# Optimization experiments

Measured on AMD Instinct MI355X. Metric: run time of the kernel, lower is better.

Reference implementation:

```python
import jax, jax.numpy as jnp
import numpy as np


def setup_inputs() -> dict:
    key = jax.random.key(0)
    k0, k1, k2, k3 = jax.random.split(key, 4)
    B, C_IN, H, W = 8, 256, 64, 64
    O, NUM = 256, 8  # output channels, number of regions
    mat0 = jax.random.normal(k0, (B, C_IN, H, W), dtype=jnp.float32)
    mat1 = jax.random.normal(k1, (O, C_IN, NUM), dtype=jnp.float32)  # per-region 1x1 filters (shared across batch, batch_W=1)
    mask = jax.random.uniform(k2, (NUM, H, W), dtype=jnp.float32)    # soft region weights per pixel
    Alpha = jax.random.uniform(k3, (NUM,), dtype=jnp.float32)        # per-region modulation scale
    return {"mat0": mat0, "mat1": mat1, "mask": mask, "Alpha": Alpha, "use_alpha": 1, "beta": 1}


def reference(mat0, mat1, mask, Alpha, use_alpha, beta):
    # Deformable (region-aware) matmul: for each pixel (h,w), apply the
    # region-r filter mat1[:, :, r] to mat0[:, :, h, w], weighted by the
    # per-pixel soft region mask (optionally alpha-modulated per region).
    # out[b,o,h,w] = sum_r sum_c mat0[b,c,h,w] * mat1[o,c,r] * Alpha[r] * mask[r,h,w]
    m1 = mat1 * Alpha if use_alpha else mat1  # [O, C, R] scaled per region
    return jnp.einsum('bchw,ocr,rhw->bohw', mat0, m1, mask)
```

## Files before the change

kernel.cpp:

```cpp
#include <hip/hip_runtime.h>
#include <hip/hip_bf16.h>
#include <stdint.h>


typedef __attribute__((ext_vector_type(8))) short short8;
typedef __attribute__((ext_vector_type(4))) float f32x4;

#define C_IN  256
#define HW_   4096
#define O_DIM 256
#define BM    128
#define BN    128
#define NRND  32

__device__ __forceinline__ short f2bf(float x) {
  union { __hip_bfloat16 h; short s; } u;
  u.h = __float2bfloat16(x);
  return u.s;
}

__global__ __launch_bounds__(256) void prep_w_kernel(
    const float* __restrict__ mat1, const float* __restrict__ Alpha,
    const int* __restrict__ use_alpha, short* __restrict__ Aprep) {
  int t = blockIdx.x * 256 + threadIdx.x;
  int o = t & 255;
  int c = t >> 8;
  int ua = use_alpha[0];
  const float* src = mat1 + ((size_t)o * C_IN + c) * 8;
  short8 v;
#pragma unroll
  for (int r = 0; r < 8; ++r) {
    float s = ua ? Alpha[r] : 1.0f;
    v[r] = f2bf(src[r] * s);
  }
  *(short8*)(Aprep + ((size_t)c * 256 + o) * 8) = v;
}

__global__ __launch_bounds__(256, 2) void gemm_deform_kernel(
    const float* __restrict__ mat0, const short* __restrict__ Aprep,
    const float* __restrict__ mask, float* __restrict__ out) {
  int bid = blockIdx.x;
  int wg = (bid & 7) * 64 + (bid >> 3);
  int tile_m = wg & 1;
  int tile_n = wg >> 1;
  int o0 = tile_m * BM;
  int n0 = tile_n * BN;
  int b  = n0 >> 12;
  int p0 = n0 & 4095;

  int t    = threadIdx.x;
  int lane = t & 63;
  int w    = t >> 6;
  int wr   = w >> 1, wc = w & 1;
  int kp   = lane >> 4;
  int li   = lane & 15;

  int colb = p0 + wc * 64 + li;
  float mk[4][8];
#pragma unroll
  for (int ni = 0; ni < 4; ++ni)
#pragma unroll
    for (int r = 0; r < 8; ++r)
      mk[ni][r] = mask[r * HW_ + colb + ni * 16];

  const short8* __restrict__ Ap = (const short8*)Aprep;
  int abase0 = kp * 256 + o0 + wr * 64 + li;

  const float* __restrict__ m0 = mat0 + ((size_t)b * C_IN + kp) * HW_ + colb;

  f32x4 acc[4][4];
#pragma unroll
  for (int mi = 0; mi < 4; ++mi)
#pragma unroll
    for (int ni = 0; ni < 4; ++ni) acc[mi][ni] = (f32x4){0.f, 0.f, 0.f, 0.f};

  short8 afA[2][4], afB[2][4];
  float  m0A[2][4], m0B[2][4];

  auto LOAD = [&](short8 (&af)[2][4], float (&m0v)[2][4], int rd) {
    int ab = rd * 8 * 256 + abase0;
#pragma unroll
    for (int ks = 0; ks < 2; ++ks)
#pragma unroll
      for (int mi = 0; mi < 4; ++mi)
        af[ks][mi] = Ap[ab + ks * 4 * 256 + mi * 16];
    const float* mp = m0 + (size_t)(rd * 8) * HW_;
#pragma unroll
    for (int ks = 0; ks < 2; ++ks)
#pragma unroll
      for (int ni = 0; ni < 4; ++ni)
        m0v[ks][ni] = mp[(size_t)(ks * 4) * HW_ + ni * 16];
  };

  auto COMP = [&](const short8 (&af)[2][4], const float (&m0v)[2][4]) {
#pragma unroll
    for (int ks = 0; ks < 2; ++ks) {
      short8 bv[4];
#pragma unroll
      for (int ni = 0; ni < 4; ++ni)
#pragma unroll
        for (int r = 0; r < 8; ++r)
          bv[ni][r] = f2bf(m0v[ks][ni] * mk[ni][r]);
#pragma unroll
      for (int mi = 0; mi < 4; ++mi)
#pragma unroll
        for (int ni = 0; ni < 4; ++ni)
          acc[mi][ni] = __builtin_amdgcn_mfma_f32_16x16x32_bf16(
              af[ks][mi], bv[ni], acc[mi][ni], 0, 0, 0);
    }
  };

  LOAD(afA, m0A, 0);
#pragma unroll 1
  for (int rd = 0; rd < NRND; rd += 2) {
    LOAD(afB, m0B, rd + 1);
    COMP(afA, m0A);
    if (rd + 2 < NRND) LOAD(afA, m0A, rd + 2);
    COMP(afB, m0B);
  }

  size_t obase = (size_t)b * O_DIM * HW_ + p0;
#pragma unroll
  for (int mi = 0; mi < 4; ++mi) {
#pragma unroll
    for (int ni = 0; ni < 4; ++ni) {
      int col = wc * 64 + ni * 16 + li;
#pragma unroll
      for (int j = 0; j < 4; ++j) {
        int row = o0 + wr * 64 + mi * 16 + kp * 4 + j;
        out[obase + (size_t)row * HW_ + col] = acc[mi][ni][j];
      }
    }
  }
}

extern "C" void kernel_launch(void* const* d_in, const int* in_sizes, int n_in,
                              void* d_out, int out_size, void* d_ws, size_t ws_size,
                              hipStream_t stream) {
  const float* mat0      = (const float*)d_in[0];
  const float* mat1      = (const float*)d_in[1];
  const float* mask      = (const float*)d_in[2];
  const float* Alpha     = (const float*)d_in[3];
  const int*   use_alpha = (const int*)d_in[4];
  (void)in_sizes; (void)n_in; (void)out_size; (void)ws_size;

  short* Aprep = (short*)d_ws;
  float* outp  = (float*)d_out;

  prep_w_kernel<<<256, 256, 0, stream>>>(mat1, Alpha, use_alpha, Aprep);
  gemm_deform_kernel<<<512, 256, 0, stream>>>(mat0, Aprep, mask, outp);
}
```

Baseline: 53.27 us.

## Split K across wave pairs with 32x32 MFMA and LDS reduction

The GEMM block grows from 256 to 512 threads. Each pair of waves splits the K dimension and uses 32x32x16 bf16 MFMAs in place of 16x16x32, with partial sums combined through shared memory before the store. This roughly halves per-wave accumulator and register pressure and doubles the waves available to hide latency. It adds a 64KB LDS reduction buffer and a block-wide barrier, and the large LDS footprint may limit how many blocks fit per CU.

```diff
diff --git a/kernel.cpp b/kernel.cpp
--- a/kernel.cpp
+++ b/kernel.cpp
@@ -3,8 +3,9 @@
 #include <stdint.h>
 
 
-typedef __attribute__((ext_vector_type(8))) short short8;
-typedef __attribute__((ext_vector_type(4))) float f32x4;
+typedef __attribute__((ext_vector_type(8)))  short short8;
+typedef __attribute__((ext_vector_type(4)))  float f32x4;
+typedef __attribute__((ext_vector_type(16))) float f32x16;
 
 #define C_IN  256
 #define HW_   4096
@@ -36,9 +37,11 @@
   *(short8*)(Aprep + ((size_t)c * 256 + o) * 8) = v;
 }
 
-__global__ __launch_bounds__(256, 2) void gemm_deform_kernel(
+__global__ __launch_bounds__(512, 4) void gemm_deform_kernel(
     const float* __restrict__ mat0, const short* __restrict__ Aprep,
     const float* __restrict__ mask, float* __restrict__ out) {
+  __shared__ float red[8 * 2048];
+
   int bid = blockIdx.x;
   int wg = (bid & 7) * 64 + (bid >> 3);
   int tile_m = wg & 1;
@@ -51,62 +54,67 @@
   int t    = threadIdx.x;
   int lane = t & 63;
   int w    = t >> 6;
-  int wr   = w >> 1, wc = w & 1;
-  int kp   = lane >> 4;
-  int li   = lane & 15;
+  int wk   = w & 1;
+  int wc   = (w >> 1) & 1;
+  int wr   = w >> 2;
+  int l31  = lane & 31;
+  int cr   = lane >> 5;
 
-  int colb = p0 + wc * 64 + li;
-  float mk[4][8];
+  int colb = p0 + wc * 64 + l31;
+  float mk[2][8];
 #pragma unroll
-  for (int ni = 0; ni < 4; ++ni)
+  for (int ni = 0; ni < 2; ++ni)
 #pragma unroll
     for (int r = 0; r < 8; ++r)
-      mk[ni][r] = mask[r * HW_ + colb + ni * 16];
+      mk[ni][r] = mask[r * HW_ + colb + ni * 32];
 
   const short8* __restrict__ Ap = (const short8*)Aprep;
-  int abase0 = kp * 256 + o0 + wr * 64 + li;
+  int abase0 = (wk * 4 + cr) * 256 + o0 + wr * 64 + l31;
 
-  const float* __restrict__ m0 = mat0 + ((size_t)b * C_IN + kp) * HW_ + colb;
+  const float* __restrict__ m0 =
+      mat0 + ((size_t)b * C_IN + wk * 4 + cr) * HW_ + colb;
 
-  f32x4 acc[4][4];
+  f32x16 acc[2][2];
 #pragma unroll
-  for (int mi = 0; mi < 4; ++mi)
+  for (int mi = 0; mi < 2; ++mi)
 #pragma unroll
-    for (int ni = 0; ni < 4; ++ni) acc[mi][ni] = (f32x4){0.f, 0.f, 0.f, 0.f};
+    for (int ni = 0; ni < 2; ++ni)
+#pragma unroll
+      for (int j = 0; j < 16; ++j) acc[mi][ni][j] = 0.f;
 
-  short8 afA[2][4], afB[2][4];
-  float  m0A[2][4], m0B[2][4];
+  short8 afA[2][2], afB[2][2];
+  float  m0A[2][2], m0B[2][2];
 
-  auto LOAD = [&](short8 (&af)[2][4], float (&m0v)[2][4], int rd) {
+  auto LOAD = [&](short8 (&af)[2][2], float (&m0v)[2][2], int rd) {
     int ab = rd * 8 * 256 + abase0;
 #pragma unroll
-    for (int ks = 0; ks < 2; ++ks)
+    for (int kq = 0; kq < 2; ++kq)
 #pragma unroll
-      for (int mi = 0; mi < 4; ++mi)
-        af[ks][mi] = Ap[ab + ks * 4 * 256 + mi * 16];
+      for (int mi = 0; mi < 2; ++mi)
+        af[kq][mi] = Ap[ab + kq * 2 * 256 + mi * 32];
     const float* mp = m0 + (size_t)(rd * 8) * HW_;
 #pragma unroll
-    for (int ks = 0; ks < 2; ++ks)
+    for (int kq = 0; kq < 2; ++kq)
 #pragma unroll
-      for (int ni = 0; ni < 4; ++ni)
-        m0v[ks][ni] = mp[(size_t)(ks * 4) * HW_ + ni * 16];
+      for (int ni = 0; ni < 2; ++ni)
+        m0v[kq][ni] = mp[(size_t)(kq * 2) * HW_ + ni * 32];
   };
 
-  auto COMP = [&](const short8 (&af)[2][4], const float (&m0v)[2][4]) {
+  auto COMP = [&](const short8 (&af)[2][2], const float (&m0v)[2][2]) {
 #pragma unroll
-    for (int ks = 0; ks < 2; ++ks) {
-      short8 bv[4];
+    for (int kq = 0; kq < 2; ++kq) {
+      short8 bv[2];
 #pragma unroll
-      for (int ni = 0; ni < 4; ++ni)
+      for (int ni = 0; ni < 2; ++ni)
 #pragma unroll
         for (int r = 0; r < 8; ++r)
-          bv[ni][r] = f2bf(m0v[ks][ni] * mk[ni][r]);
+          bv[ni][r] = f2bf(m0v[kq][ni] * mk[ni][r]);
 #pragma unroll
-      for (int mi = 0; mi < 4; ++mi)
+      for (int mi = 0; mi < 2; ++mi)
 #pragma unroll
-        for (int ni = 0; ni < 4; ++ni)
-          acc[mi][ni] = __builtin_amdgcn_mfma_f32_16x16x32_bf16(
-              af[ks][mi], bv[ni], acc[mi][ni], 0, 0, 0);
+        for (int ni = 0; ni < 2; ++ni)
+          acc[mi][ni] = __builtin_amdgcn_mfma_f32_32x32x16_bf16(
+              af[kq][mi], bv[ni], acc[mi][ni], 0, 0, 0);
     }
   };
 
@@ -119,17 +127,36 @@
     COMP(afB, m0B);
   }
 
+  int pairid = wr * 2 + wc;
+  int other  = wk ^ 1;
+  float* reg_w = &red[(pairid * 2 + other) * 2048];
+#pragma unroll
+  for (int ni = 0; ni < 2; ++ni)
+#pragma unroll
+    for (int q = 0; q < 4; ++q) {
+      f32x4 v;
+#pragma unroll
+      for (int j = 0; j < 4; ++j) v[j] = acc[other][ni][q * 4 + j];
+      *(f32x4*)&reg_w[(q * 128 + ni * 64 + lane) * 4] = v;
+    }
+  __syncthreads();
+
+  const float* reg_r = &red[(pairid * 2 + wk) * 2048];
   size_t obase = (size_t)b * O_DIM * HW_ + p0;
 #pragma unroll
-  for (int mi = 0; mi < 4; ++mi) {
+  for (int ni = 0; ni < 2; ++ni) {
+    f32x16 s = acc[wk][ni];
 #pragma unroll
-    for (int ni = 0; ni < 4; ++ni) {
-      int col = wc * 64 + ni * 16 + li;
+    for (int q = 0; q < 4; ++q) {
+      f32x4 v = *(const f32x4*)&reg_r[(q * 128 + ni * 64 + lane) * 4];
 #pragma unroll
-      for (int j = 0; j < 4; ++j) {
-        int row = o0 + wr * 64 + mi * 16 + kp * 4 + j;
-        out[obase + (size_t)row * HW_ + col] = acc[mi][ni][j];
-      }
+      for (int j = 0; j < 4; ++j) s[q * 4 + j] += v[j];
+    }
+    int col = wc * 64 + ni * 32 + l31;
+#pragma unroll
+    for (int reg = 0; reg < 16; ++reg) {
+      int row = o0 + wr * 64 + wk * 32 + (reg & 3) + 8 * (reg >> 2) + 4 * cr;
+      out[obase + (size_t)row * HW_ + col] = s[reg];
     }
   }
 }
@@ -148,5 +175,5 @@
   float* outp  = (float*)d_out;
 
   prep_w_kernel<<<256, 256, 0, stream>>>(mat1, Alpha, use_alpha, Aprep);
-  gemm_deform_kernel<<<512, 256, 0, stream>>>(mat0, Aprep, mask, outp);
+  gemm_deform_kernel<<<512, 512, 0, stream>>>(mat0, Aprep, mask, outp);
 }
```

New measurement: 93.40 us. +75.3%, slower.

## Switch to 32x32x16 MFMA with 8-wave blocks and rolling prefetch

Applied to the files above, without the earlier changes.

Replaces the 16x16x32 bf16 MFMA tiling with 32x32x16 MFMA and doubles the block to 512 threads (8 waves, 4x2 layout), so each wave owns a 64x32 output tile. Each lane now computes a single mask column, which cuts the mask registers and the bf16 conversion work per MFMA. The A-double-buffer is replaced by a per-k-step rolling prefetch into the same registers. The intent is higher MFMA efficiency and occupancy from lower register use. In exchange each wave does less reuse per loaded element, and the output stores use a different access pattern.

```diff
diff --git a/kernel.cpp b/kernel.cpp
--- a/kernel.cpp
+++ b/kernel.cpp
@@ -3,14 +3,11 @@
 #include <stdint.h>
 
 
-typedef __attribute__((ext_vector_type(8))) short short8;
-typedef __attribute__((ext_vector_type(4))) float f32x4;
+typedef __attribute__((ext_vector_type(8)))  short short8;
+typedef __attribute__((ext_vector_type(16))) float f32x16;
 
 #define C_IN  256
 #define HW_   4096
-#define O_DIM 256
-#define BM    128
-#define BN    128
 #define NRND  32
 
 __device__ __forceinline__ short f2bf(float x) {
@@ -36,100 +33,86 @@
   *(short8*)(Aprep + ((size_t)c * 256 + o) * 8) = v;
 }
 
-__global__ __launch_bounds__(256, 2) void gemm_deform_kernel(
+__global__ __launch_bounds__(512, 4) void gemm_deform_kernel(
     const float* __restrict__ mat0, const short* __restrict__ Aprep,
     const float* __restrict__ mask, float* __restrict__ out) {
   int bid = blockIdx.x;
   int wg = (bid & 7) * 64 + (bid >> 3);
   int tile_m = wg & 1;
   int tile_n = wg >> 1;
-  int o0 = tile_m * BM;
-  int n0 = tile_n * BN;
+  int o0 = tile_m * 128;
+  int n0 = tile_n * 128;
   int b  = n0 >> 12;
   int p0 = n0 & 4095;
 
   int t    = threadIdx.x;
   int lane = t & 63;
   int w    = t >> 6;
-  int wr   = w >> 1, wc = w & 1;
-  int kp   = lane >> 4;
-  int li   = lane & 15;
+  int wc   = w & 3;
+  int wr   = w >> 2;
+  int l31  = lane & 31;
+  int cr   = lane >> 5;
 
-  int colb = p0 + wc * 64 + li;
-  float mk[4][8];
+  int col = p0 + wc * 32 + l31;
+  float mk[8];
 #pragma unroll
-  for (int ni = 0; ni < 4; ++ni)
-#pragma unroll
-    for (int r = 0; r < 8; ++r)
-      mk[ni][r] = mask[r * HW_ + colb + ni * 16];
+  for (int r = 0; r < 8; ++r) mk[r] = mask[r * HW_ + col];
 
   const short8* __restrict__ Ap = (const short8*)Aprep;
-  int abase0 = kp * 256 + o0 + wr * 64 + li;
+  int aoff = cr * 256 + o0 + wr * 64 + l31;
 
-  const float* __restrict__ m0 = mat0 + ((size_t)b * C_IN + kp) * HW_ + colb;
+  const float* __restrict__ m0b =
+      mat0 + ((size_t)b * C_IN + cr) * HW_ + col;
 
-  f32x4 acc[4][4];
+  f32x16 acc[2];
 #pragma unroll
-  for (int mi = 0; mi < 4; ++mi)
+  for (int mi = 0; mi < 2; ++mi)
 #pragma unroll
-    for (int ni = 0; ni < 4; ++ni) acc[mi][ni] = (f32x4){0.f, 0.f, 0.f, 0.f};
+    for (int j = 0; j < 16; ++j) acc[mi][j] = 0.f;
 
-  short8 afA[2][4], afB[2][4];
-  float  m0A[2][4], m0B[2][4];
+  short8 af[4][2];
+  float  P[4];
 
-  auto LOAD = [&](short8 (&af)[2][4], float (&m0v)[2][4], int rd) {
-    int ab = rd * 8 * 256 + abase0;
 #pragma unroll
-    for (int ks = 0; ks < 2; ++ks)
+  for (int kq = 0; kq < 4; ++kq) {
 #pragma unroll
-      for (int mi = 0; mi < 4; ++mi)
-        af[ks][mi] = Ap[ab + ks * 4 * 256 + mi * 16];
-    const float* mp = m0 + (size_t)(rd * 8) * HW_;
-#pragma unroll
-    for (int ks = 0; ks < 2; ++ks)
-#pragma unroll
-      for (int ni = 0; ni < 4; ++ni)
-        m0v[ks][ni] = mp[(size_t)(ks * 4) * HW_ + ni * 16];
-  };
-
-  auto COMP = [&](const short8 (&af)[2][4], const float (&m0v)[2][4]) {
-#pragma unroll
-    for (int ks = 0; ks < 2; ++ks) {
-      short8 bv[4];
-#pragma unroll
-      for (int ni = 0; ni < 4; ++ni)
-#pragma unroll
-        for (int r = 0; r < 8; ++r)
-          bv[ni][r] = f2bf(m0v[ks][ni] * mk[ni][r]);
-#pragma unroll
-      for (int mi = 0; mi < 4; ++mi)
-#pragma unroll
-        for (int ni = 0; ni < 4; ++ni)
-          acc[mi][ni] = __builtin_amdgcn_mfma_f32_16x16x32_bf16(
-              af[ks][mi], bv[ni], acc[mi][ni], 0, 0, 0);
-    }
-  };
-
-  LOAD(afA, m0A, 0);
-#pragma unroll 1
-  for (int rd = 0; rd < NRND; rd += 2) {
-    LOAD(afB, m0B, rd + 1);
-    COMP(afA, m0A);
-    if (rd + 2 < NRND) LOAD(afA, m0A, rd + 2);
-    COMP(afB, m0B);
+    for (int mi = 0; mi < 2; ++mi)
+      af[kq][mi] = Ap[aoff + kq * 512 + mi * 32];
+    P[kq] = m0b[(size_t)(kq * 2) * HW_];
   }
 
-  size_t obase = (size_t)b * O_DIM * HW_ + p0;
+#pragma unroll 1
+  for (int rd = 0; rd < NRND - 1; ++rd) {
+    int abase = (rd + 1) * 2048 + aoff;
+    const float* mnext = m0b + (size_t)((rd + 1) * 8) * HW_;
 #pragma unroll
-  for (int mi = 0; mi < 4; ++mi) {
+    for (int kq = 0; kq < 4; ++kq) {
+      short8 bv;
 #pragma unroll
-    for (int ni = 0; ni < 4; ++ni) {
-      int col = wc * 64 + ni * 16 + li;
+      for (int r = 0; r < 8; ++r) bv[r] = f2bf(P[kq] * mk[r]);
+      acc[0] = __builtin_amdgcn_mfma_f32_32x32x16_bf16(af[kq][0], bv, acc[0], 0, 0, 0);
+      acc[1] = __builtin_amdgcn_mfma_f32_32x32x16_bf16(af[kq][1], bv, acc[1], 0, 0, 0);
+      af[kq][0] = Ap[abase + kq * 512];
+      af[kq][1] = Ap[abase + kq * 512 + 32];
+      P[kq] = mnext[(size_t)(kq * 2) * HW_];
+    }
+  }
 #pragma unroll
-      for (int j = 0; j < 4; ++j) {
-        int row = o0 + wr * 64 + mi * 16 + kp * 4 + j;
-        out[obase + (size_t)row * HW_ + col] = acc[mi][ni][j];
-      }
+  for (int kq = 0; kq < 4; ++kq) {
+    short8 bv;
+#pragma unroll
+    for (int r = 0; r < 8; ++r) bv[r] = f2bf(P[kq] * mk[r]);
+    acc[0] = __builtin_amdgcn_mfma_f32_32x32x16_bf16(af[kq][0], bv, acc[0], 0, 0, 0);
+    acc[1] = __builtin_amdgcn_mfma_f32_32x32x16_bf16(af[kq][1], bv, acc[1], 0, 0, 0);
+  }
+
+  size_t obase = (size_t)b * 256 * HW_ + col;
+#pragma unroll
+  for (int mi = 0; mi < 2; ++mi) {
+#pragma unroll
+    for (int reg = 0; reg < 16; ++reg) {
+      int row = o0 + wr * 64 + mi * 32 + (reg & 3) + 8 * (reg >> 2) + 4 * cr;
+      out[obase + (size_t)row * HW_] = acc[mi][reg];
     }
   }
 }
@@ -148,5 +131,5 @@
   float* outp  = (float*)d_out;
 
   prep_w_kernel<<<256, 256, 0, stream>>>(mat1, Alpha, use_alpha, Aprep);
-  gemm_deform_kernel<<<512, 256, 0, stream>>>(mat0, Aprep, mask, outp);
+  gemm_deform_kernel<<<512, 512, 0, stream>>>(mat0, Aprep, mask, outp);
 }
```

After: 57.41 us. 7.8% more time.
